# Performance work log

Measured on AMD Instinct MI355X. Metric: run time of the kernel, lower is better.

Reference implementation:

```python
import jax, jax.numpy as jnp
import numpy as np

NUM_EMBEDDINGS = 512
EMBEDDING_DIM = 64


def setup_inputs() -> dict:
    key = jax.random.key(0)
    k1, k2 = jax.random.split(key)
    z = jax.random.normal(k1, (4, EMBEDDING_DIM, 16, 64, 64), dtype=jnp.float32)
    # embedding init: uniform(-1/K, 1/K)
    bound = 1.0 / NUM_EMBEDDINGS
    emb_weight = jax.random.uniform(k2, (NUM_EMBEDDINGS, EMBEDDING_DIM),
                                    dtype=jnp.float32, minval=-bound, maxval=bound)
    return {"z": z, "emb_weight": emb_weight}


def reference(z, emb_weight):
    # z: [B, C, D, H, W] with C == embedding_dim
    B, C, D, H, W = z.shape
    z_perm = jnp.transpose(z, (0, 2, 3, 4, 1))          # [B, D, H, W, C]
    flat_z = z_perm.reshape(-1, C)                       # [N, C]
    distances = (jnp.sum(flat_z * flat_z, axis=1, keepdims=True)
                 - 2.0 * flat_z @ emb_weight.T
                 + jnp.sum(emb_weight * emb_weight, axis=1))  # [N, K]
    encoding_indices = jnp.argmin(distances, axis=1)     # [N]
    # jit-safe unique count: number of codebook entries used at least once
    counts = jnp.zeros((emb_weight.shape[0],), dtype=jnp.int32).at[encoding_indices].add(1)
    unique_codes = jnp.sum(counts > 0)
    z_q = emb_weight[encoding_indices].reshape(z_perm.shape)  # [B, D, H, W, C]
    # straight-through estimator
    z_q = z_perm + jax.lax.stop_gradient(z_q - z_perm)
    z_q = jnp.transpose(z_q, (0, 4, 1, 2, 3))            # [B, C, D, H, W]
    return z_q, unique_codes
```

## Files before the change

### kernel.cpp

```cpp
#include <hip/hip_runtime.h>
#include <hip/hip_bf16.h>

#define NPOS (4*16*64*64)
#define KCODES 512
#define CDIM 64
#define OUT_SCALAR_IDX ((size_t)NPOS * CDIM)

#define WS_GCOUNT 0
#define WS_EMB    4096
#define WS_EE     (4096 + 32768)

typedef float f32x4 __attribute__((ext_vector_type(4)));
typedef long lng2 __attribute__((ext_vector_type(2)));

__global__ __launch_bounds__(64) void vq_prep(
    const float* __restrict__ emb, char* __restrict__ ws) {
  const int r = blockIdx.x * 64 + threadIdx.x;
  ((int*)(ws + WS_GCOUNT))[r] = 0;
  float c[CDIM];
  float ee = 0.f;
  #pragma unroll
  for (int q = 0; q < 16; ++q) {
    float4 x = ((const float4*)(emb + r * CDIM))[q];
    c[4*q+0] = x.x; c[4*q+1] = x.y; c[4*q+2] = x.z; c[4*q+3] = x.w;
    ee = fmaf(x.x, x.x, ee); ee = fmaf(x.y, x.y, ee);
    ee = fmaf(x.z, x.z, ee); ee = fmaf(x.w, x.w, ee);
  }
  #pragma unroll
  for (int kg = 0; kg < 4; ++kg) {
    uint u[4];
    #pragma unroll
    for (int h = 0; h < 2; ++h)
      #pragma unroll
      for (int jj = 0; jj < 2; ++jj) {
        const int kb = h * 32 + kg * 8 + jj * 4;
        uint p = __builtin_amdgcn_cvt_pk_fp8_f32(-512.f * c[kb+0], -512.f * c[kb+1], 0u, false);
        p = __builtin_amdgcn_cvt_pk_fp8_f32(-512.f * c[kb+2], -512.f * c[kb+3], p, true);
        u[h * 2 + jj] = p;
      }
    *(uint4*)(ws + WS_EMB + kg * 8192 + r * 16) = make_uint4(u[0], u[1], u[2], u[3]);
  }
  ((float*)(ws + WS_EE))[r] = 256.f * (1.f + ee);
}

__global__ __launch_bounds__(512, 4) void vq_mfma(
    const float* __restrict__ z, const float* __restrict__ emb,
    const char* __restrict__ ws, float* __restrict__ out,
    int* __restrict__ gflags) {
  __shared__ lng2 embs[2048];
  __shared__ float s_ee[KCODES];
  __shared__ uint s_idx[512];
  __shared__ int s_hist[KCODES];

  const int tid = threadIdx.x;
  const int lane = tid & 63;
  const int w = tid >> 6;
  const int col = lane & 15;
  const int kg = lane >> 4;

  if (tid < 128)
    __builtin_amdgcn_global_load_lds(
        (const __attribute__((address_space(1))) void*)(ws + WS_EE + tid * 16),
        (__attribute__((address_space(3))) void*)((char*)s_ee + tid * 16), 16, 0, 0);
  const char* src = ws + WS_EMB;
  #pragma unroll
  for (int i = 0; i < 4; ++i) {
    const int off = (i * 512 + tid) * 16;
    __builtin_amdgcn_global_load_lds(
        (const __attribute__((address_space(1))) void*)(src + off),
        (__attribute__((address_space(3))) void*)((char*)embs + off), 16, 0, 0);
  }

  const int nb = blockIdx.x * 512;
  const int b = nb >> 16, spb = nb & 65535;
  const float* zp0 = z + ((size_t)b << 22) + spb;
  const int pbase = w * 32 + col;

  float pf0[32], pf1[32];
  #pragma unroll
  for (int rt = 0; rt < 2; ++rt)
    #pragma unroll
    for (int h = 0; h < 2; ++h)
      #pragma unroll
      for (int j = 0; j < 8; ++j)
        pf0[rt*16 + h*8 + j] =
            zp0[pbase + rt*16 + ((size_t)(h*32 + kg*8 + j) << 16)];
  #pragma unroll
  for (int rt = 0; rt < 2; ++rt)
    #pragma unroll
    for (int h = 0; h < 2; ++h)
      #pragma unroll
      for (int j = 0; j < 8; ++j)
        pf1[rt*16 + h*8 + j] =
            zp0[256 + pbase + rt*16 + ((size_t)(h*32 + kg*8 + j) << 16)];

  long af0[2][2];
  #pragma unroll
  for (int rt = 0; rt < 2; ++rt)
    #pragma unroll
    for (int h = 0; h < 2; ++h) {
      const int o = rt*16 + h*8;
      uint u0 = __builtin_amdgcn_cvt_pk_fp8_f32(pf0[o+0], pf0[o+1], 0u, false);
      u0 = __builtin_amdgcn_cvt_pk_fp8_f32(pf0[o+2], pf0[o+3], u0, true);
      uint u1 = __builtin_amdgcn_cvt_pk_fp8_f32(pf0[o+4], pf0[o+5], 0u, false);
      u1 = __builtin_amdgcn_cvt_pk_fp8_f32(pf0[o+6], pf0[o+7], u1, true);
      af0[rt][h] = ((long)u1 << 32) | (long)u0;
    }
  s_hist[tid] = 0;

  asm volatile("s_waitcnt vmcnt(32) lgkmcnt(0)" ::: "memory");
  __builtin_amdgcn_sched_barrier(0);
  __builtin_amdgcn_s_barrier();
  __builtin_amdgcn_sched_barrier(0);

  const int lbyte = kg * 8192 + col * 16;

#define CHUNK(AF, SBASE)                                                       \
  {                                                                            \
    uint key[2][4];                                                            \
    _Pragma("unroll") for (int rt = 0; rt < 2; ++rt)                           \
      _Pragma("unroll") for (int s = 0; s < 4; ++s) key[rt][s] = 0xFFFFFFFFu;  \
    lng2 bb = *(const lng2*)((const char*)embs + lbyte);                       \
    float eev = s_ee[col];                                                     \
    _Pragma("unroll 8")                                                        \
    for (int ct = 0; ct < 32; ++ct) {                                          \
      const lng2 bc = bb;                                                      \
      const float ec = eev;                                                    \
      const uint ctv = (uint)ct;                                               \
      const int nct = (ct + 1) & 31;                                           \
      bb = *(const lng2*)((const char*)embs + nct * 256 + lbyte);              \
      eev = s_ee[nct * 16 + col];                                              \
      const f32x4 cin = {ec, ec, ec, ec};                                      \
      _Pragma("unroll") for (int rt = 0; rt < 2; ++rt) {                       \
        f32x4 acc =                                                            \
            __builtin_amdgcn_mfma_f32_16x16x32_fp8_fp8(AF[rt][0], bc.x, cin, 0, 0, 0); \
        acc = __builtin_amdgcn_mfma_f32_16x16x32_fp8_fp8(AF[rt][1], bc.y, acc, 0, 0, 0); \
        _Pragma("unroll") for (int s = 0; s < 4; ++s) {                        \
          uint kb = (__builtin_bit_cast(uint, acc[s]) & 0xFFFFFFE0u) | ctv;    \
          key[rt][s] = kb < key[rt][s] ? kb : key[rt][s];                      \
        }                                                                      \
      }                                                                        \
    }                                                                          \
    _Pragma("unroll") for (int rt = 0; rt < 2; ++rt)                           \
      _Pragma("unroll") for (int s = 0; s < 4; ++s) {                          \
        uint k = (key[rt][s] << 4) | (uint)col;                                \
        _Pragma("unroll") for (int m = 1; m < 16; m <<= 1) {                   \
          uint o = (uint)__shfl_xor((int)k, m, 64);                            \
          k = o < k ? o : k;                                                   \
        }                                                                      \
        if (col == 0) s_idx[(SBASE) + w * 32 + rt * 16 + kg * 4 + s] = k;      \
      }                                                                        \
  }

  CHUNK(af0, 0)

  long af1[2][2];
  #pragma unroll
  for (int rt = 0; rt < 2; ++rt)
    #pragma unroll
    for (int h = 0; h < 2; ++h) {
      const int o = rt*16 + h*8;
      uint u0 = __builtin_amdgcn_cvt_pk_fp8_f32(pf1[o+0], pf1[o+1], 0u, false);
      u0 = __builtin_amdgcn_cvt_pk_fp8_f32(pf1[o+2], pf1[o+3], u0, true);
      uint u1 = __builtin_amdgcn_cvt_pk_fp8_f32(pf1[o+4], pf1[o+5], 0u, false);
      u1 = __builtin_amdgcn_cvt_pk_fp8_f32(pf1[o+6], pf1[o+7], u1, true);
      af1[rt][h] = ((long)u1 << 32) | (long)u0;
    }

  CHUNK(af1, 256)

  __syncthreads();

  const uint kk = s_idx[tid];
  const int myidx = (int)(((kk >> 4) & 31u) * 16u + (kk & 15u));
  atomicAdd(&s_hist[myidx], 1);
  {
    const float4* ef = (const float4*)(emb + myidx * CDIM);
    float* o = out + ((size_t)b << 22) + spb + tid;
    #pragma unroll
    for (int q = 0; q < 16; ++q) {
      float4 e4 = ef[q];
      o[(size_t)(4 * q + 0) << 16] = e4.x;
      o[(size_t)(4 * q + 1) << 16] = e4.y;
      o[(size_t)(4 * q + 2) << 16] = e4.z;
      o[(size_t)(4 * q + 3) << 16] = e4.w;
    }
  }
  __syncthreads();
  if (s_hist[tid]) gflags[tid] = 1;
}

__global__ __launch_bounds__(512) void vq_count(
    const int* __restrict__ gflags, float* __restrict__ out) {
  __shared__ int red[512];
  const int t = threadIdx.x;
  red[t] = (gflags[t] > 0) ? 1 : 0;
  __syncthreads();
  for (int s = 256; s > 0; s >>= 1) {
    if (t < s) red[t] += red[t + s];
    __syncthreads();
  }
  if (t == 0) out[OUT_SCALAR_IDX] = (float)red[0];
}

extern "C" void kernel_launch(void* const* d_in, const int* in_sizes, int n_in,
                              void* d_out, int out_size, void* d_ws, size_t ws_size,
                              hipStream_t stream) {
  const float* z = (const float*)d_in[0];
  const float* emb = (const float*)d_in[1];
  float* out = (float*)d_out;
  char* ws = (char*)d_ws;
  int* gflags = (int*)(ws + WS_GCOUNT);

  vq_prep<<<8, 64, 0, stream>>>(emb, ws);
  vq_mfma<<<NPOS / 512, 512, 0, stream>>>(z, emb, ws, out, gflags);
  vq_count<<<1, 512, 0, stream>>>(gflags, out);
}
```

Before: 39.28 us.

## Pipeline z loads across four chunks and fuse unique-count into main kernel

Result: slower. 154.7 us (+293.8%).

```diff
diff --git a/kernel.cpp b/kernel.cpp
--- a/kernel.cpp
+++ b/kernel.cpp
@@ -1,14 +1,14 @@
 #include <hip/hip_runtime.h>
-#include <hip/hip_bf16.h>
 
 #define NPOS (4*16*64*64)
 #define KCODES 512
 #define CDIM 64
 #define OUT_SCALAR_IDX ((size_t)NPOS * CDIM)
 
-#define WS_GCOUNT 0
-#define WS_EMB    4096
-#define WS_EE     (4096 + 32768)
+#define WS_MASK  0
+#define WS_FCNT  64
+#define WS_EMB   4096
+#define WS_EE    (4096 + 32768)
 
 typedef float f32x4 __attribute__((ext_vector_type(4)));
 typedef long lng2 __attribute__((ext_vector_type(2)));
@@ -16,7 +16,7 @@
 __global__ __launch_bounds__(64) void vq_prep(
     const float* __restrict__ emb, char* __restrict__ ws) {
   const int r = blockIdx.x * 64 + threadIdx.x;
-  ((int*)(ws + WS_GCOUNT))[r] = 0;
+  if (r < 17) ((int*)(ws + WS_MASK))[r] = 0;
   float c[CDIM];
   float ee = 0.f;
   #pragma unroll
@@ -45,18 +45,21 @@
 
 __global__ __launch_bounds__(512, 4) void vq_mfma(
     const float* __restrict__ z, const float* __restrict__ emb,
-    const char* __restrict__ ws, float* __restrict__ out,
-    int* __restrict__ gflags) {
+    char* __restrict__ ws, float* __restrict__ out) {
   __shared__ lng2 embs[2048];
   __shared__ float s_ee[KCODES];
   __shared__ uint s_idx[512];
-  __shared__ int s_hist[KCODES];
+  __shared__ uint s_mask[16];
+  __shared__ int s_red[16];
+  __shared__ int s_last;
 
   const int tid = threadIdx.x;
   const int lane = tid & 63;
   const int w = tid >> 6;
   const int col = lane & 15;
   const int kg = lane >> 4;
+
+  if (tid < 16) s_mask[tid] = 0;
 
   if (tid < 128)
     __builtin_amdgcn_global_load_lds(
@@ -73,53 +76,34 @@
 
   const int nb = blockIdx.x * 512;
   const int b = nb >> 16, spb = nb & 65535;
-  const float* zp0 = z + ((size_t)b << 22) + spb;
-  const int pbase = w * 32 + col;
-
-  float pf0[32], pf1[32];
-  #pragma unroll
-  for (int rt = 0; rt < 2; ++rt)
-    #pragma unroll
-    for (int h = 0; h < 2; ++h)
-      #pragma unroll
-      for (int j = 0; j < 8; ++j)
-        pf0[rt*16 + h*8 + j] =
-            zp0[pbase + rt*16 + ((size_t)(h*32 + kg*8 + j) << 16)];
-  #pragma unroll
-  for (int rt = 0; rt < 2; ++rt)
-    #pragma unroll
-    for (int h = 0; h < 2; ++h)
-      #pragma unroll
-      for (int j = 0; j < 8; ++j)
-        pf1[rt*16 + h*8 + j] =
-            zp0[256 + pbase + rt*16 + ((size_t)(h*32 + kg*8 + j) << 16)];
-
-  long af0[2][2];
-  #pragma unroll
-  for (int rt = 0; rt < 2; ++rt)
-    #pragma unroll
-    for (int h = 0; h < 2; ++h) {
-      const int o = rt*16 + h*8;
-      uint u0 = __builtin_amdgcn_cvt_pk_fp8_f32(pf0[o+0], pf0[o+1], 0u, false);
-      u0 = __builtin_amdgcn_cvt_pk_fp8_f32(pf0[o+2], pf0[o+3], u0, true);
-      uint u1 = __builtin_amdgcn_cvt_pk_fp8_f32(pf0[o+4], pf0[o+5], 0u, false);
-      u1 = __builtin_amdgcn_cvt_pk_fp8_f32(pf0[o+6], pf0[o+7], u1, true);
-      af0[rt][h] = ((long)u1 << 32) | (long)u0;
-    }
-  s_hist[tid] = 0;
-
-  asm volatile("s_waitcnt vmcnt(32) lgkmcnt(0)" ::: "memory");
-  __builtin_amdgcn_sched_barrier(0);
-  __builtin_amdgcn_s_barrier();
-  __builtin_amdgcn_sched_barrier(0);
-
+  const float* zp = z + ((size_t)b << 22) + spb + w * 16 + col;
   const int lbyte = kg * 8192 + col * 16;
 
-#define CHUNK(AF, SBASE)                                                       \
+  float pf0[16], pf1[16];
+  long afx, afy;
+
+#define ISSUE(PF, C)                                                           \
+  _Pragma("unroll") for (int h = 0; h < 2; ++h)                                \
+  _Pragma("unroll") for (int j = 0; j < 8; ++j)                                \
+    PF[h*8+j] = zp[(C)*128 + ((size_t)(h*32 + kg*8 + j) << 16)];
+
+#define CONV(PF)                                                               \
   {                                                                            \
-    uint key[2][4];                                                            \
-    _Pragma("unroll") for (int rt = 0; rt < 2; ++rt)                           \
-      _Pragma("unroll") for (int s = 0; s < 4; ++s) key[rt][s] = 0xFFFFFFFFu;  \
+    uint u0 = __builtin_amdgcn_cvt_pk_fp8_f32(PF[0], PF[1], 0u, false);        \
+    u0 = __builtin_amdgcn_cvt_pk_fp8_f32(PF[2], PF[3], u0, true);              \
+    uint u1 = __builtin_amdgcn_cvt_pk_fp8_f32(PF[4], PF[5], 0u, false);        \
+    u1 = __builtin_amdgcn_cvt_pk_fp8_f32(PF[6], PF[7], u1, true);              \
+    afx = ((long)u1 << 32) | (long)u0;                                         \
+    u0 = __builtin_amdgcn_cvt_pk_fp8_f32(PF[8], PF[9], 0u, false);             \
+    u0 = __builtin_amdgcn_cvt_pk_fp8_f32(PF[10], PF[11], u0, true);            \
+    u1 = __builtin_amdgcn_cvt_pk_fp8_f32(PF[12], PF[13], 0u, false);           \
+    u1 = __builtin_amdgcn_cvt_pk_fp8_f32(PF[14], PF[15], u1, true);            \
+    afy = ((long)u1 << 32) | (long)u0;                                         \
+  }
+
+#define HOT(C)                                                                 \
+  {                                                                            \
+    uint key[4] = {0xFFFFFFFFu, 0xFFFFFFFFu, 0xFFFFFFFFu, 0xFFFFFFFFu};        \
     lng2 bb = *(const lng2*)((const char*)embs + lbyte);                       \
     float eev = s_ee[col];                                                     \
     _Pragma("unroll 8")                                                        \
@@ -131,49 +115,47 @@
       bb = *(const lng2*)((const char*)embs + nct * 256 + lbyte);              \
       eev = s_ee[nct * 16 + col];                                              \
       const f32x4 cin = {ec, ec, ec, ec};                                      \
-      _Pragma("unroll") for (int rt = 0; rt < 2; ++rt) {                       \
-        f32x4 acc =                                                            \
-            __builtin_amdgcn_mfma_f32_16x16x32_fp8_fp8(AF[rt][0], bc.x, cin, 0, 0, 0); \
-        acc = __builtin_amdgcn_mfma_f32_16x16x32_fp8_fp8(AF[rt][1], bc.y, acc, 0, 0, 0); \
-        _Pragma("unroll") for (int s = 0; s < 4; ++s) {                        \
-          uint kb = (__builtin_bit_cast(uint, acc[s]) & 0xFFFFFFE0u) | ctv;    \
-          key[rt][s] = kb < key[rt][s] ? kb : key[rt][s];                      \
-        }                                                                      \
+      f32x4 acc = __builtin_amdgcn_mfma_f32_16x16x32_fp8_fp8(afx, bc.x, cin, 0, 0, 0); \
+      acc = __builtin_amdgcn_mfma_f32_16x16x32_fp8_fp8(afy, bc.y, acc, 0, 0, 0); \
+      _Pragma("unroll") for (int s = 0; s < 4; ++s) {                          \
+        uint kb = (__builtin_bit_cast(uint, acc[s]) & 0xFFFFFFE0u) | ctv;      \
+        key[s] = kb < key[s] ? kb : key[s];                                    \
       }                                                                        \
     }                                                                          \
-    _Pragma("unroll") for (int rt = 0; rt < 2; ++rt)                           \
-      _Pragma("unroll") for (int s = 0; s < 4; ++s) {                          \
-        uint k = (key[rt][s] << 4) | (uint)col;                                \
-        _Pragma("unroll") for (int m = 1; m < 16; m <<= 1) {                   \
-          uint o = (uint)__shfl_xor((int)k, m, 64);                            \
-          k = o < k ? o : k;                                                   \
-        }                                                                      \
-        if (col == 0) s_idx[(SBASE) + w * 32 + rt * 16 + kg * 4 + s] = k;      \
+    _Pragma("unroll") for (int s = 0; s < 4; ++s) {                            \
+      uint k = (key[s] << 4) | (uint)col;                                      \
+      _Pragma("unroll") for (int m = 1; m < 16; m <<= 1) {                     \
+        uint o = (uint)__shfl_xor((int)k, m, 64);                              \
+        k = o < k ? o : k;                                                     \
       }                                                                        \
-  }
-
-  CHUNK(af0, 0)
-
-  long af1[2][2];
-  #pragma unroll
-  for (int rt = 0; rt < 2; ++rt)
-    #pragma unroll
-    for (int h = 0; h < 2; ++h) {
-      const int o = rt*16 + h*8;
-      uint u0 = __builtin_amdgcn_cvt_pk_fp8_f32(pf1[o+0], pf1[o+1], 0u, false);
-      u0 = __builtin_amdgcn_cvt_pk_fp8_f32(pf1[o+2], pf1[o+3], u0, true);
-      uint u1 = __builtin_amdgcn_cvt_pk_fp8_f32(pf1[o+4], pf1[o+5], 0u, false);
-      u1 = __builtin_amdgcn_cvt_pk_fp8_f32(pf1[o+6], pf1[o+7], u1, true);
-      af1[rt][h] = ((long)u1 << 32) | (long)u0;
-    }
-
-  CHUNK(af1, 256)
+      if (col == 0) s_idx[(C) * 128 + w * 16 + kg * 4 + s] = k;                \
+    }                                                                          \
+  }
+
+  ISSUE(pf0, 0)
+  ISSUE(pf1, 1)
+  CONV(pf0)
+  ISSUE(pf0, 2)
+
+  asm volatile("s_waitcnt vmcnt(32) lgkmcnt(0)" ::: "memory");
+  __builtin_amdgcn_sched_barrier(0);
+  __builtin_amdgcn_s_barrier();
+  __builtin_amdgcn_sched_barrier(0);
+
+  HOT(0)
+  CONV(pf1)
+  ISSUE(pf1, 3)
+  HOT(1)
+  CONV(pf0)
+  HOT(2)
+  CONV(pf1)
+  HOT(3)
 
   __syncthreads();
 
   const uint kk = s_idx[tid];
   const int myidx = (int)(((kk >> 4) & 31u) * 16u + (kk & 15u));
-  atomicAdd(&s_hist[myidx], 1);
+  atomicOr(&s_mask[myidx >> 5], 1u << (myidx & 31));
   {
     const float4* ef = (const float4*)(emb + myidx * CDIM);
     float* o = out + ((size_t)b << 22) + spb + tid;
@@ -187,20 +169,25 @@
     }
   }
   __syncthreads();
-  if (s_hist[tid]) gflags[tid] = 1;
-}
-
-__global__ __launch_bounds__(512) void vq_count(
-    const int* __restrict__ gflags, float* __restrict__ out) {
-  __shared__ int red[512];
-  const int t = threadIdx.x;
-  red[t] = (gflags[t] > 0) ? 1 : 0;
-  __syncthreads();
-  for (int s = 256; s > 0; s >>= 1) {
-    if (t < s) red[t] += red[t + s];
+
+  uint* gmask = (uint*)(ws + WS_MASK);
+  if (tid < 16 && s_mask[tid]) atomicOr(&gmask[tid], s_mask[tid]);
+  __threadfence();
+  __syncthreads();
+  if (tid == 0)
+    s_last = (atomicAdd((int*)(ws + WS_FCNT), 1) == (int)gridDim.x - 1);
+  __syncthreads();
+  if (s_last) {
+    __threadfence();
+    if (tid < 16) s_red[tid] = __popc(atomicOr(&gmask[tid], 0u));
     __syncthreads();
-  }
-  if (t == 0) out[OUT_SCALAR_IDX] = (float)red[0];
+    if (tid == 0) {
+      int c = 0;
+      #pragma unroll
+      for (int i = 0; i < 16; ++i) c += s_red[i];
+      out[OUT_SCALAR_IDX] = (float)c;
+    }
+  }
 }
 
 extern "C" void kernel_launch(void* const* d_in, const int* in_sizes, int n_in,
@@ -210,9 +197,7 @@
   const float* emb = (const float*)d_in[1];
   float* out = (float*)d_out;
   char* ws = (char*)d_ws;
-  int* gflags = (int*)(ws + WS_GCOUNT);
 
   vq_prep<<<8, 64, 0, stream>>>(emb, ws);
-  vq_mfma<<<NPOS / 512, 512, 0, stream>>>(z, emb, ws, out, gflags);
-  vq_count<<<1, 512, 0, stream>>>(gflags, out);
+  vq_mfma<<<NPOS / 512, 512, 0, stream>>>(z, emb, ws, out);
 }
```
